# Kernel tuning notes

Hardware: AMD Instinct MI355X
Metric: run time of the kernel (lower is better)

## Reference

```python
import jax, jax.numpy as jnp
import numpy as np
import math

S, B, D, H = 1024, 4, 1024, 16
DH = D // H


def setup_inputs() -> dict:
    key = jax.random.key(0)
    ks = jax.random.split(key, 8)
    hidden_states = jax.random.normal(ks[0], (S, B, D), dtype=jnp.float32)
    u = jax.random.uniform(ks[1], (B, 1, 1, S), dtype=jnp.float32)
    attention_mask = jnp.where(u < 0.2, jnp.float32(-10000.0), jnp.float32(0.0))
    std = 0.02
    Wq = jax.random.normal(ks[2], (D, D), dtype=jnp.float32) * std
    bq = jnp.zeros((D,), dtype=jnp.float32)
    Wk = jax.random.normal(ks[3], (D, D), dtype=jnp.float32) * std
    bk = jnp.zeros((D,), dtype=jnp.float32)
    Wv = jax.random.normal(ks[4], (D, D), dtype=jnp.float32) * std
    bv = jnp.zeros((D,), dtype=jnp.float32)
    return {"hidden_states": hidden_states, "attention_mask": attention_mask,
            "Wq": Wq, "bq": bq, "Wk": Wk, "bk": bk, "Wv": Wv, "bv": bv}


def _split_heads(x):
    # [S,B,D] -> [B,H,S,DH]
    s, b, d = x.shape
    return x.reshape(s, b, H, DH).transpose(1, 2, 0, 3)


def reference(hidden_states, attention_mask, Wq, bq, Wk, bk, Wv, bv):
    scale = 1.0 / math.sqrt(DH)
    q = _split_heads(hidden_states @ Wq.T + bq)  # [B,H,S,DH]
    k = _split_heads(hidden_states @ Wk.T + bk)
    v = _split_heads(hidden_states @ Wv.T + bv)
    # scaled scores + additive mask (mask [B,1,1,S] broadcasts over heads, query pos)
    scores = jnp.einsum('bhsd,bhtd->bhst', q, k) * scale + attention_mask  # [B,H,S,S]
    probs = jax.nn.softmax(scores, axis=-1)
    # NOTE: original forward's dropout block is a no-op (only reshapes), so none applied
    ctx = jnp.einsum('bhst,bhtd->bhsd', probs, v)  # [B,H,S,DH]
    # -> [S,B,D]
    return ctx.transpose(2, 0, 1, 3).reshape(S, B, D)
```

## Files before the change

kernel.cpp:

```cpp
#include <hip/hip_runtime.h>
#include <hip/hip_bf16.h>

#define S_LEN  1024
#define BATCH  4
#define DMODEL 1024
#define NHEAD  16
#define DHEAD  64
#define NROWS  (S_LEN*BATCH)

typedef __bf16 bf16;
typedef __bf16 bf16x2 __attribute__((ext_vector_type(2)));
typedef __bf16 bf16x4 __attribute__((ext_vector_type(4)));
typedef __bf16 bf16x8 __attribute__((ext_vector_type(8)));
typedef float  f32x4  __attribute__((ext_vector_type(4)));
typedef float  f32x16 __attribute__((ext_vector_type(16)));

#define AS1 __attribute__((address_space(1)))
#define AS3 __attribute__((address_space(3)))

#define QSCALE  0.18033688011112042f

__device__ __forceinline__ void gload16(const bf16* g, bf16* l) {
  __builtin_amdgcn_global_load_lds((const AS1 void*)g, (AS3 void*)l, 16, 0, 0);
}

__device__ __forceinline__ float fast_exp2(float x) {
#if __has_builtin(__builtin_amdgcn_exp2f)
  return __builtin_amdgcn_exp2f(x);
#else
  return exp2f(x);
#endif
}

__global__ __launch_bounds__(256) void cvt_all(
    const float* __restrict__ hs, const float* __restrict__ wq,
    const float* __restrict__ wk, const float* __restrict__ wv,
    const float* __restrict__ mask,
    bf16* __restrict__ Xb, bf16* __restrict__ Wb,
    unsigned long long* __restrict__ mbits)
{
  const int b = blockIdx.x;
  if (b == 3584) {
    const int wv = threadIdx.x >> 6, lane = threadIdx.x & 63;
    #pragma unroll
    for (int t16 = 0; t16 < 16; ++t16) {
      const float v = mask[(size_t)wv*S_LEN + t16*64 + lane];
      const unsigned long long bal = __ballot(v < -1000.f);
      if (lane == 0) mbits[wv*16 + t16] = bal;
    }
    return;
  }
  const float* src; bf16* dst; int i;
  if (b < 2048)      { src = hs; dst = Xb;                           i = b*256        + threadIdx.x; }
  else if (b < 2560) { src = wq; dst = Wb;                           i = (b-2048)*256 + threadIdx.x; }
  else if (b < 3072) { src = wk; dst = Wb + (size_t)DMODEL*DMODEL;   i = (b-2560)*256 + threadIdx.x; }
  else               { src = wv; dst = Wb + (size_t)2*DMODEL*DMODEL; i = (b-3072)*256 + threadIdx.x; }
  const float4* s4 = (const float4*)src;
  float4 a = s4[2*i], c = s4[2*i+1];
  bf16x8 o;
  o[0]=(bf16)a.x; o[1]=(bf16)a.y; o[2]=(bf16)a.z; o[3]=(bf16)a.w;
  o[4]=(bf16)c.x; o[5]=(bf16)c.y; o[6]=(bf16)c.z; o[7]=(bf16)c.w;
  ((bf16x8*)dst)[i] = o;
}

#define BM 128
#define BN 128
#define BK 32

__global__ __launch_bounds__(256) void qkv_gemm(
    const bf16* __restrict__ X, const bf16* __restrict__ Wcat,
    const float* __restrict__ bq, const float* __restrict__ bk, const float* __restrict__ bv,
    bf16* __restrict__ Qo, bf16* __restrict__ Ko, bf16* __restrict__ Vo)
{
  __shared__ __align__(16) bf16 As[BM*BK];
  __shared__ __align__(16) bf16 Bs[BN*BK];

  const int tid  = threadIdx.x;
  const int row0 = blockIdx.x * BM;
  const int col0 = blockIdx.y * BN;
  const int wsel = col0 >> 10;
  const int coln = col0 & 1023;

  const int wv   = tid >> 6;
  const int lane = tid & 63;
  const int lg   = lane >> 4;
  const int lr   = lane & 15;
  const int wr   = (wv >> 1) << 6;
  const int wc   = (wv & 1) << 6;

  const int c0 = tid, c1 = tid + 256;
  const size_t gA0 = (size_t)(row0 + (c0>>2))*DMODEL + (size_t)((c0&3)<<3);
  const size_t gA1 = (size_t)(row0 + (c1>>2))*DMODEL + (size_t)((c1&3)<<3);
  const size_t gB0 = (size_t)(col0 + (c0>>2))*DMODEL + (size_t)((c0&3)<<3);
  const size_t gB1 = (size_t)(col0 + (c1>>2))*DMODEL + (size_t)((c1&3)<<3);
  const int wb = (tid >> 6) << 6;
  bf16* lA0 = As + (size_t)wb*8;
  bf16* lA1 = As + (size_t)(wb+256)*8;
  bf16* lB0 = Bs + (size_t)wb*8;
  bf16* lB1 = Bs + (size_t)(wb+256)*8;

  f32x4 acc[4][4];
  #pragma unroll
  for (int mi=0; mi<4; ++mi)
    #pragma unroll
    for (int ni=0; ni<4; ++ni)
      acc[mi][ni] = (f32x4){0.f,0.f,0.f,0.f};

  for (int k0 = 0; k0 < DMODEL; k0 += BK) {
    __syncthreads();
    gload16(X    + gA0 + k0, lA0);
    gload16(X    + gA1 + k0, lA1);
    gload16(Wcat + gB0 + k0, lB0);
    gload16(Wcat + gB1 + k0, lB1);
    __syncthreads();

    bf16x8 af[4], bfr[4];
    #pragma unroll
    for (int mi=0; mi<4; ++mi)
      af[mi] = *(const bf16x8*)&As[(wr + mi*16 + lr)*BK + lg*8];
    #pragma unroll
    for (int ni=0; ni<4; ++ni)
      bfr[ni] = *(const bf16x8*)&Bs[(wc + ni*16 + lr)*BK + lg*8];

    #pragma unroll
    for (int mi=0; mi<4; ++mi)
      #pragma unroll
      for (int ni=0; ni<4; ++ni)
        acc[mi][ni] = __builtin_amdgcn_mfma_f32_16x16x32_bf16(af[mi], bfr[ni], acc[mi][ni], 0, 0, 0);
  }

  const float* bias = (wsel==0) ? bq : ((wsel==1) ? bk : bv);
  bf16* Out = (wsel==0) ? Qo : ((wsel==1) ? Ko : Vo);
  const float oscale = (wsel==0) ? QSCALE : 1.0f;

  #pragma unroll
  for (int ni=0; ni<4; ++ni) {
    const int co = coln + wc + ni*16 + lr;
    const float bias_v = bias[co];
    const int h  = co >> 6;
    const int dh = co & 63;
    #pragma unroll
    for (int mi=0; mi<4; ++mi) {
      #pragma unroll
      for (int p=0; p<4; ++p) {
        const int gr = row0 + wr + mi*16 + lg*4 + p;
        const int s_ = gr >> 2;
        const int b_ = gr & 3;
        Out[((size_t)(b_*NHEAD + h)*S_LEN + s_)*DHEAD + dh] = (bf16)((acc[mi][ni][p] + bias_v) * oscale);
      }
    }
  }
}

__global__ __launch_bounds__(256) void vtrans(const bf16* __restrict__ V, bf16* __restrict__ VT)
{
  __shared__ bf16 Ts[64][72];
  const int bh = blockIdx.x;
  const int s0 = blockIdx.y * 64;
  const int tid = threadIdx.x;
  const int r = tid >> 2, c = (tid & 3) << 4;
  const bf16* src = V + ((size_t)bh*S_LEN + s0 + r)*DHEAD + c;
  *(bf16x8*)&Ts[r][c]     = *(const bf16x8*)src;
  *(bf16x8*)&Ts[r][c + 8] = *(const bf16x8*)(src + 8);
  __syncthreads();
  const int d = tid >> 2, sc = (tid & 3) << 4;
  bf16x8 o0, o1;
  #pragma unroll
  for (int i=0;i<8;++i) { o0[i] = Ts[sc+i][d]; o1[i] = Ts[sc+8+i][d]; }
  bf16* dst = VT + ((size_t)bh*DHEAD + d)*S_LEN + s0 + sc;
  *(bf16x8*)dst       = o0;
  *(bf16x8*)(dst + 8) = o1;
}

#define QBLK 128
#define KVB  64
#define LSWK(row, chunk) (((row)<<6) + ((((chunk) ^ ((row)&7)))<<3))

__global__ __launch_bounds__(256, 4) void attn_mfma(
    const bf16* __restrict__ Q, const bf16* __restrict__ K, const bf16* __restrict__ VT,
    const unsigned long long* __restrict__ mbits, float* __restrict__ out)
{
  __shared__ __align__(16) bf16 KsBuf[2][KVB*64];
  __shared__ __align__(16) bf16 VtBuf[2][64*KVB];
  __shared__ float Linv[4][32];

  const int bh   = blockIdx.x;
  const int b_   = bh >> 4;
  const int h_   = bh & 15;
  const int tid  = threadIdx.x;
  const int wv   = tid >> 6;
  const int lane = tid & 63;
  const int l31  = lane & 31;
  const int hh   = lane >> 5;
  const int q0   = blockIdx.y * QBLK;

  const bf16* Qp = Q + ((size_t)bh*S_LEN + q0 + wv*32 + l31)*DHEAD;
  bf16x8 qb[4];
  #pragma unroll
  for (int dk=0; dk<4; ++dk) qb[dk] = *(const bf16x8*)&Qp[dk*16 + hh*8];

  const bf16* Kb  = K  + (size_t)bh*S_LEN*DHEAD;
  const bf16* VTb = VT + (size_t)bh*DHEAD*S_LEN;
  const unsigned long long* mbp = mbits + (size_t)b_*16;

  const int g0   = wv*64 + lane;
  const int row0_= g0 >> 3, cs0 = g0 & 7;
  const int ch0  = cs0 ^ (row0_ & 7);
  const size_t koff0 = (size_t)row0_*DHEAD + ch0*8;
  const size_t koff1 = koff0 + (size_t)32*DHEAD;
  const size_t voff0 = (size_t)row0_*S_LEN + ch0*8;
  const size_t voff1 = voff0 + (size_t)32*S_LEN;
  bf16* kd0 = (bf16*)KsBuf[0];
  bf16* vd0 = (bf16*)VtBuf[0];
  const int wdst0 = wv*512, wdst1 = wv*512 + 2048;

  gload16(Kb  + koff0,  kd0 + wdst0);
  gload16(Kb  + koff1,  kd0 + wdst1);
  gload16(VTb + voff0,  vd0 + wdst0);
  gload16(VTb + voff1,  vd0 + wdst1);
  __syncthreads();

  f32x16 ctx[2];
  ctx[0] = (f32x16)0.f; ctx[1] = (f32x16)0.f;
  float lsum = 0.f;

  for (int t = 0; t < 16; ++t) {
    const bf16* Kc = KsBuf[t & 1];
    const bf16* Vc = VtBuf[t & 1];

    if (t < 15) {
      const size_t nk = (size_t)(t+1)*KVB*DHEAD;
      const size_t nv = (size_t)(t+1)*KVB;
      bf16* kn = (bf16*)KsBuf[(t+1) & 1];
      bf16* vn = (bf16*)VtBuf[(t+1) & 1];
      gload16(Kb  + nk + koff0, kn + wdst0);
      gload16(Kb  + nk + koff1, kn + wdst1);
      gload16(VTb + nv + voff0, vn + wdst0);
      gload16(VTb + nv + voff1, vn + wdst1);
    }

    const unsigned long long mt = mbp[t];

    #pragma unroll
    for (int t2=0; t2<2; ++t2) {
      f32x16 sacc = (f32x16)0.f;
      const int row = t2*32 + l31;
      __builtin_amdgcn_s_setprio(1);
      #pragma unroll
      for (int dk=0; dk<4; ++dk) {
        bf16x8 ka = *(const bf16x8*)&Kc[LSWK(row, dk*2 + hh)];
        sacc = __builtin_amdgcn_mfma_f32_32x32x16_bf16(ka, qb[dk], sacc, 0,0,0);
      }
      __builtin_amdgcn_s_setprio(0);

      const unsigned int mw = (unsigned int)(mt >> (t2*32 + 4*hh));
      float pe[16];
      #pragma unroll
      for (int e=0; e<16; ++e) {
        const float ex = fast_exp2(sacc[e]);
        pe[e] = ((mw >> ((e&3) + 8*(e>>2))) & 1u) ? 0.f : ex;
        lsum += pe[e];
      }
      bf16x8 pf[2];
      {
        union { bf16x2 h2[8]; bf16x8 v[2]; } u;
        #pragma unroll
        for (int j=0; j<8; ++j) { bf16x2 p2; p2[0]=(bf16)pe[2*j]; p2[1]=(bf16)pe[2*j+1]; u.h2[j]=p2; }
        pf[0] = u.v[0]; pf[1] = u.v[1];
      }

      __builtin_amdgcn_s_setprio(1);
      #pragma unroll
      for (int nt=0; nt<2; ++nt) {
        const int drow = nt*32 + l31;
        const int dbase = (drow<<6) + 4*hh;
        const int dsw = (drow&7);
        #pragma unroll
        for (int kk=0; kk<2; ++kk) {
          const int lc = t2*4 + kk*2;
          bf16x4 lo = *(const bf16x4*)&Vc[dbase + (((lc  ) ^ dsw)<<3)];
          bf16x4 hi = *(const bf16x4*)&Vc[dbase + (((lc+1) ^ dsw)<<3)];
          bf16x8 vb;
          #pragma unroll
          for (int j=0; j<4; ++j) { vb[j]=lo[j]; vb[4+j]=hi[j]; }
          ctx[nt] = __builtin_amdgcn_mfma_f32_32x32x16_bf16(pf[kk], vb, ctx[nt], 0,0,0);
        }
      }
      __builtin_amdgcn_s_setprio(0);
    }

    __syncthreads();
  }

  const float tot = lsum + __shfl_xor(lsum, 32);
  if (lane < 32) Linv[wv][l31] = 1.f / tot;
  f32x4 inv4[4];
  #pragma unroll
  for (int g4=0; g4<4; ++g4) inv4[g4] = *(const f32x4*)&Linv[wv][8*g4 + 4*hh];

  float* op = out + ((size_t)(q0 + wv*32)*BATCH + b_)*DMODEL + h_*DHEAD + l31;
  #pragma unroll
  for (int e=0; e<16; ++e) {
    const int qe = (e&3) + 8*(e>>2) + 4*hh;
    const float inv = inv4[e>>2][e&3];
    float* oq = op + (size_t)qe*BATCH*DMODEL;
    oq[0]  = ctx[0][e] * inv;
    oq[32] = ctx[1][e] * inv;
  }
}

extern "C" void kernel_launch(void* const* d_in, const int* in_sizes, int n_in,
                              void* d_out, int out_size, void* d_ws, size_t ws_size,
                              hipStream_t stream) {
  const float* hs   = (const float*)d_in[0];
  const float* mask = (const float*)d_in[1];
  const float* Wq   = (const float*)d_in[2];
  const float* bq   = (const float*)d_in[3];
  const float* Wk   = (const float*)d_in[4];
  const float* bk   = (const float*)d_in[5];
  const float* Wv   = (const float*)d_in[6];
  const float* bv   = (const float*)d_in[7];
  float* out = (float*)d_out;

  char* ws = (char*)d_ws;
  bf16* Xb = (bf16*)ws;
  bf16* Wb = Xb + (size_t)NROWS*DMODEL;
  bf16* Qw = Wb + (size_t)3*DMODEL*DMODEL;
  bf16* Kw = Qw + (size_t)NROWS*DMODEL;
  bf16* Vw = Kw + (size_t)NROWS*DMODEL;
  unsigned long long* Mb = (unsigned long long*)(Vw + (size_t)NROWS*DMODEL);
  bf16* VTw = Xb;

  cvt_all<<<3585, 256, 0, stream>>>(hs, Wq, Wk, Wv, mask, Xb, Wb, Mb);

  qkv_gemm<<<dim3(NROWS/BM, 3*DMODEL/BN), 256, 0, stream>>>(Xb, Wb, bq, bk, bv, Qw, Kw, Vw);

  vtrans<<<dim3(BATCH*NHEAD, S_LEN/64), 256, 0, stream>>>(Vw, VTw);

  attn_mfma<<<dim3(BATCH*NHEAD, S_LEN/QBLK), 256, 0, stream>>>(Qw, Kw, VTw, Mb, out);
}
```

Measured before the change: 80.82 us.

## Split attention over two KV halves with a combine kernel and XCD-aware block mapping

Attention is split along the key dimension into two halves, doubling the grid from 512 to 1024 blocks to fill more CUs. The block ids are remapped so that each head's blocks fall on the same XCD, which is meant to improve L2 reuse of K and V. A new combine kernel adds the two partial contexts, stored as bf16, and normalizes them by the summed row totals. This works without max rescaling only because the softmax has no running max. In exchange it adds an extra kernel launch, a round trip of the partial results through global memory, and some precision loss from storing partials in bf16. The original kernel is kept as a fallback when the workspace is too small.

```diff
diff --git a/kernel.cpp b/kernel.cpp
--- a/kernel.cpp
+++ b/kernel.cpp
@@ -176,59 +176,63 @@
 #define KVB  64
 #define LSWK(row, chunk) (((row)<<6) + ((((chunk) ^ ((row)&7)))<<3))
 
-__global__ __launch_bounds__(256, 4) void attn_mfma(
+__global__ __launch_bounds__(256, 4) void attn_split(
     const bf16* __restrict__ Q, const bf16* __restrict__ K, const bf16* __restrict__ VT,
-    const unsigned long long* __restrict__ mbits, float* __restrict__ out)
+    const unsigned long long* __restrict__ mbits,
+    bf16* __restrict__ Pc, float* __restrict__ Pl)
 {
   __shared__ __align__(16) bf16 KsBuf[2][KVB*64];
   __shared__ __align__(16) bf16 VtBuf[2][64*KVB];
-  __shared__ float Linv[4][32];
-
-  const int bh   = blockIdx.x;
+
+  const int id   = blockIdx.x;
+  const int xcd  = id & 7;
+  const int rank = id >> 3;
+  const int bh   = xcd*8 + (rank >> 4);
+  const int r2   = rank & 15;
+  const int qb   = r2 >> 1;
+  const int sp   = r2 & 1;
+
   const int b_   = bh >> 4;
-  const int h_   = bh & 15;
   const int tid  = threadIdx.x;
   const int wv   = tid >> 6;
   const int lane = tid & 63;
   const int l31  = lane & 31;
   const int hh   = lane >> 5;
-  const int q0   = blockIdx.y * QBLK;
+  const int q0   = qb * QBLK;
 
   const bf16* Qp = Q + ((size_t)bh*S_LEN + q0 + wv*32 + l31)*DHEAD;
-  bf16x8 qb[4];
-  #pragma unroll
-  for (int dk=0; dk<4; ++dk) qb[dk] = *(const bf16x8*)&Qp[dk*16 + hh*8];
+  bf16x8 qb_[4];
+  #pragma unroll
+  for (int dk=0; dk<4; ++dk) qb_[dk] = *(const bf16x8*)&Qp[dk*16 + hh*8];
 
   const bf16* Kb  = K  + (size_t)bh*S_LEN*DHEAD;
   const bf16* VTb = VT + (size_t)bh*DHEAD*S_LEN;
-  const unsigned long long* mbp = mbits + (size_t)b_*16;
+  const unsigned long long* mbp = mbits + (size_t)b_*16 + sp*8;
 
   const int g0   = wv*64 + lane;
   const int row0_= g0 >> 3, cs0 = g0 & 7;
   const int ch0  = cs0 ^ (row0_ & 7);
-  const size_t koff0 = (size_t)row0_*DHEAD + ch0*8;
+  const size_t koff0 = (size_t)row0_*DHEAD + ch0*8 + (size_t)sp*8*KVB*DHEAD;
   const size_t koff1 = koff0 + (size_t)32*DHEAD;
-  const size_t voff0 = (size_t)row0_*S_LEN + ch0*8;
+  const size_t voff0 = (size_t)row0_*S_LEN + ch0*8 + (size_t)sp*8*KVB;
   const size_t voff1 = voff0 + (size_t)32*S_LEN;
-  bf16* kd0 = (bf16*)KsBuf[0];
-  bf16* vd0 = (bf16*)VtBuf[0];
   const int wdst0 = wv*512, wdst1 = wv*512 + 2048;
 
-  gload16(Kb  + koff0,  kd0 + wdst0);
-  gload16(Kb  + koff1,  kd0 + wdst1);
-  gload16(VTb + voff0,  vd0 + wdst0);
-  gload16(VTb + voff1,  vd0 + wdst1);
+  gload16(Kb  + koff0,  (bf16*)KsBuf[0] + wdst0);
+  gload16(Kb  + koff1,  (bf16*)KsBuf[0] + wdst1);
+  gload16(VTb + voff0,  (bf16*)VtBuf[0] + wdst0);
+  gload16(VTb + voff1,  (bf16*)VtBuf[0] + wdst1);
   __syncthreads();
 
   f32x16 ctx[2];
   ctx[0] = (f32x16)0.f; ctx[1] = (f32x16)0.f;
   float lsum = 0.f;
 
-  for (int t = 0; t < 16; ++t) {
+  for (int t = 0; t < 8; ++t) {
     const bf16* Kc = KsBuf[t & 1];
     const bf16* Vc = VtBuf[t & 1];
 
-    if (t < 15) {
+    if (t < 7) {
       const size_t nk = (size_t)(t+1)*KVB*DHEAD;
       const size_t nv = (size_t)(t+1)*KVB;
       bf16* kn = (bf16*)KsBuf[(t+1) & 1];
@@ -249,7 +253,7 @@
       #pragma unroll
       for (int dk=0; dk<4; ++dk) {
         bf16x8 ka = *(const bf16x8*)&Kc[LSWK(row, dk*2 + hh)];
-        sacc = __builtin_amdgcn_mfma_f32_32x32x16_bf16(ka, qb[dk], sacc, 0,0,0);
+        sacc = __builtin_amdgcn_mfma_f32_32x32x16_bf16(ka, qb_[dk], sacc, 0,0,0);
       }
       __builtin_amdgcn_s_setprio(0);
 
@@ -293,6 +297,160 @@
   }
 
   const float tot = lsum + __shfl_xor(lsum, 32);
+  if (lane < 32) Pl[(size_t)(sp*64 + bh)*S_LEN + q0 + wv*32 + l31] = tot;
+
+  bf16* pc = Pc + ((size_t)(sp*64 + bh)*S_LEN + q0 + wv*32)*DHEAD + l31;
+  #pragma unroll
+  for (int e=0; e<16; ++e) {
+    const int qe = (e&3) + 8*(e>>2) + 4*hh;
+    bf16* pq = pc + (size_t)qe*DHEAD;
+    pq[0]  = (bf16)ctx[0][e];
+    pq[32] = (bf16)ctx[1][e];
+  }
+}
+
+__global__ __launch_bounds__(256) void attn_combine(
+    const bf16* __restrict__ Pc, const float* __restrict__ Pl, float* __restrict__ out)
+{
+  const int bh = blockIdx.x;
+  const int b_ = bh >> 4;
+  const int h_ = bh & 15;
+  const int tid = threadIdx.x;
+  const int q  = blockIdx.y*128 + (tid >> 1);
+  const int d0 = (tid & 1) << 5;
+
+  const size_t i0 = ((size_t)bh*S_LEN + q)*DHEAD + d0;
+  const size_t i1 = ((size_t)(64 + bh)*S_LEN + q)*DHEAD + d0;
+  bf16x8 a0[4], a1[4];
+  #pragma unroll
+  for (int j=0; j<4; ++j) { a0[j] = *(const bf16x8*)&Pc[i0 + j*8]; a1[j] = *(const bf16x8*)&Pc[i1 + j*8]; }
+  const float l0 = Pl[(size_t)bh*S_LEN + q];
+  const float l1 = Pl[(size_t)(64 + bh)*S_LEN + q];
+  const float inv = 1.f / (l0 + l1);
+
+  float* op = out + ((size_t)q*BATCH + b_)*DMODEL + h_*DHEAD + d0;
+  #pragma unroll
+  for (int j=0; j<4; ++j) {
+    f32x4 o0, o1;
+    #pragma unroll
+    for (int k=0; k<4; ++k) {
+      o0[k] = ((float)a0[j][k]   + (float)a1[j][k])   * inv;
+      o1[k] = ((float)a0[j][4+k] + (float)a1[j][4+k]) * inv;
+    }
+    *(f32x4*)&op[j*8]     = o0;
+    *(f32x4*)&op[j*8 + 4] = o1;
+  }
+}
+
+__global__ __launch_bounds__(256, 4) void attn_mfma(
+    const bf16* __restrict__ Q, const bf16* __restrict__ K, const bf16* __restrict__ VT,
+    const unsigned long long* __restrict__ mbits, float* __restrict__ out)
+{
+  __shared__ __align__(16) bf16 KsBuf[2][KVB*64];
+  __shared__ __align__(16) bf16 VtBuf[2][64*KVB];
+  __shared__ float Linv[4][32];
+
+  const int bh   = blockIdx.x;
+  const int b_   = bh >> 4;
+  const int h_   = bh & 15;
+  const int tid  = threadIdx.x;
+  const int wv   = tid >> 6;
+  const int lane = tid & 63;
+  const int l31  = lane & 31;
+  const int hh   = lane >> 5;
+  const int q0   = blockIdx.y * QBLK;
+
+  const bf16* Qp = Q + ((size_t)bh*S_LEN + q0 + wv*32 + l31)*DHEAD;
+  bf16x8 qb[4];
+  #pragma unroll
+  for (int dk=0; dk<4; ++dk) qb[dk] = *(const bf16x8*)&Qp[dk*16 + hh*8];
+
+  const bf16* Kb  = K  + (size_t)bh*S_LEN*DHEAD;
+  const bf16* VTb = VT + (size_t)bh*DHEAD*S_LEN;
+  const unsigned long long* mbp = mbits + (size_t)b_*16;
+
+  const int g0   = wv*64 + lane;
+  const int row0_= g0 >> 3, cs0 = g0 & 7;
+  const int ch0  = cs0 ^ (row0_ & 7);
+  const size_t koff0 = (size_t)row0_*DHEAD + ch0*8;
+  const size_t koff1 = koff0 + (size_t)32*DHEAD;
+  const size_t voff0 = (size_t)row0_*S_LEN + ch0*8;
+  const size_t voff1 = voff0 + (size_t)32*S_LEN;
+  const int wdst0 = wv*512, wdst1 = wv*512 + 2048;
+
+  gload16(Kb  + koff0,  (bf16*)KsBuf[0] + wdst0);
+  gload16(Kb  + koff1,  (bf16*)KsBuf[0] + wdst1);
+  gload16(VTb + voff0,  (bf16*)VtBuf[0] + wdst0);
+  gload16(VTb + voff1,  (bf16*)VtBuf[0] + wdst1);
+  __syncthreads();
+
+  f32x16 ctx[2];
+  ctx[0] = (f32x16)0.f; ctx[1] = (f32x16)0.f;
+  float lsum = 0.f;
+
+  for (int t = 0; t < 16; ++t) {
+    const bf16* Kc = KsBuf[t & 1];
+    const bf16* Vc = VtBuf[t & 1];
+    if (t < 15) {
+      const size_t nk = (size_t)(t+1)*KVB*DHEAD;
+      const size_t nv = (size_t)(t+1)*KVB;
+      bf16* kn = (bf16*)KsBuf[(t+1) & 1];
+      bf16* vn = (bf16*)VtBuf[(t+1) & 1];
+      gload16(Kb  + nk + koff0, kn + wdst0);
+      gload16(Kb  + nk + koff1, kn + wdst1);
+      gload16(VTb + nv + voff0, vn + wdst0);
+      gload16(VTb + nv + voff1, vn + wdst1);
+    }
+    const unsigned long long mt = mbp[t];
+    #pragma unroll
+    for (int t2=0; t2<2; ++t2) {
+      f32x16 sacc = (f32x16)0.f;
+      const int row = t2*32 + l31;
+      __builtin_amdgcn_s_setprio(1);
+      #pragma unroll
+      for (int dk=0; dk<4; ++dk) {
+        bf16x8 ka = *(const bf16x8*)&Kc[LSWK(row, dk*2 + hh)];
+        sacc = __builtin_amdgcn_mfma_f32_32x32x16_bf16(ka, qb[dk], sacc, 0,0,0);
+      }
+      __builtin_amdgcn_s_setprio(0);
+      const unsigned int mw = (unsigned int)(mt >> (t2*32 + 4*hh));
+      float pe[16];
+      #pragma unroll
+      for (int e=0; e<16; ++e) {
+        const float ex = fast_exp2(sacc[e]);
+        pe[e] = ((mw >> ((e&3) + 8*(e>>2))) & 1u) ? 0.f : ex;
+        lsum += pe[e];
+      }
+      bf16x8 pf[2];
+      {
+        union { bf16x2 h2[8]; bf16x8 v[2]; } u;
+        #pragma unroll
+        for (int j=0; j<8; ++j) { bf16x2 p2; p2[0]=(bf16)pe[2*j]; p2[1]=(bf16)pe[2*j+1]; u.h2[j]=p2; }
+        pf[0] = u.v[0]; pf[1] = u.v[1];
+      }
+      __builtin_amdgcn_s_setprio(1);
+      #pragma unroll
+      for (int nt=0; nt<2; ++nt) {
+        const int drow = nt*32 + l31;
+        const int dbase = (drow<<6) + 4*hh;
+        const int dsw = (drow&7);
+        #pragma unroll
+        for (int kk=0; kk<2; ++kk) {
+          const int lc = t2*4 + kk*2;
+          bf16x4 lo = *(const bf16x4*)&Vc[dbase + (((lc  ) ^ dsw)<<3)];
+          bf16x4 hi = *(const bf16x4*)&Vc[dbase + (((lc+1) ^ dsw)<<3)];
+          bf16x8 vb;
+          #pragma unroll
+          for (int j=0; j<4; ++j) { vb[j]=lo[j]; vb[4+j]=hi[j]; }
+          ctx[nt] = __builtin_amdgcn_mfma_f32_32x32x16_bf16(pf[kk], vb, ctx[nt], 0,0,0);
+        }
+      }
+      __builtin_amdgcn_s_setprio(0);
+    }
+    __syncthreads();
+  }
+
+  const float tot = lsum + __shfl_xor(lsum, 32);
   if (lane < 32) Linv[wv][l31] = 1.f / tot;
   f32x4 inv4[4];
   #pragma unroll
@@ -329,13 +487,22 @@
   bf16* Kw = Qw + (size_t)NROWS*DMODEL;
   bf16* Vw = Kw + (size_t)NROWS*DMODEL;
   unsigned long long* Mb = (unsigned long long*)(Vw + (size_t)NROWS*DMODEL);
+  bf16*  Pc = (bf16*)((char*)Mb + 4096);
+  float* Pl = (float*)(Pc + (size_t)2*64*S_LEN*DHEAD);
   bf16* VTw = Xb;
 
+  const size_t need = ((char*)(Pl + (size_t)2*64*S_LEN) - ws);
+
   cvt_all<<<3585, 256, 0, stream>>>(hs, Wq, Wk, Wv, mask, Xb, Wb, Mb);
 
   qkv_gemm<<<dim3(NROWS/BM, 3*DMODEL/BN), 256, 0, stream>>>(Xb, Wb, bq, bk, bv, Qw, Kw, Vw);
 
   vtrans<<<dim3(BATCH*NHEAD, S_LEN/64), 256, 0, stream>>>(Vw, VTw);
 
-  attn_mfma<<<dim3(BATCH*NHEAD, S_LEN/QBLK), 256, 0, stream>>>(Qw, Kw, VTw, Mb, out);
-}
+  if (ws_size >= need) {
+    attn_split<<<1024, 256, 0, stream>>>(Qw, Kw, VTw, Mb, Pc, Pl);
+    attn_combine<<<dim3(BATCH*NHEAD, S_LEN/128), 256, 0, stream>>>(Pc, Pl, out);
+  } else {
+    attn_mfma<<<dim3(BATCH*NHEAD, S_LEN/QBLK), 256, 0, stream>>>(Qw, Kw, VTw, Mb, out);
+  }
+}
```

Measured after the change: 88.22 us. 9.2% more time.
